# Performance work log

Measured on AMD Instinct MI355X. Metric: run time of the kernel, lower is better.

## Reference

```python
import jax, jax.numpy as jnp
import numpy as np

NUM_HEADS = 16
DIM_K = 64
EMB_DIM = 1024
NEG_INF = -1.0e9


def setup_inputs() -> dict:
    key = jax.random.key(0)
    ks = jax.random.split(key, 12)
    B, Sq, Skv, D = 2, 2048, 2048, EMB_DIM
    HDK = NUM_HEADS * DIM_K
    s = 1.0 / np.sqrt(D)
    return {
        "q": jax.random.normal(ks[0], (B, Sq, D), jnp.float32),
        "k": jax.random.normal(ks[1], (B, Skv, D), jnp.float32),
        "v": jax.random.normal(ks[2], (B, Skv, D), jnp.float32),
        "mask": jax.random.randint(ks[3], (B, 1, Skv), 0, 2, jnp.int32),
        "Wq": jax.random.normal(ks[4], (D, HDK), jnp.float32) * s,
        "bq": jnp.zeros((HDK,), jnp.float32),
        "Wk": jax.random.normal(ks[5], (D, HDK), jnp.float32) * s,
        "bk": jnp.zeros((HDK,), jnp.float32),
        "Wv": jax.random.normal(ks[6], (D, HDK), jnp.float32) * s,
        "bv": jnp.zeros((HDK,), jnp.float32),
        "Wo": jax.random.normal(ks[7], (HDK, D), jnp.float32) * (1.0 / np.sqrt(HDK)),
        "bo": jnp.zeros((D,), jnp.float32),
    }


def reference(q, k, v, mask, Wq, bq, Wk, bk, Wv, bv, Wo, bo):
    B, Sq, _ = q.shape
    Skv = k.shape[1]
    H, dk = NUM_HEADS, DIM_K
    # projections  (B,S,D) -> (B,H,S,dk)
    qh = (q @ Wq + bq).reshape(B, Sq, H, dk).transpose(0, 2, 1, 3)
    kh = (k @ Wk + bk).reshape(B, Skv, H, dk).transpose(0, 2, 1, 3)
    vh = (v @ Wv + bv).reshape(B, Skv, H, dk).transpose(0, 2, 1, 3)
    # scores (B,H,Sq,Skv)
    scores = jnp.einsum("bhqd,bhkd->bhqk", qh, kh) / jnp.float32(np.sqrt(dk))
    # mask (B,1,Skv) -> (B,1,1,Skv); masked_fill where mask == 0
    scores = jnp.where(mask[:, None] == 0, jnp.float32(NEG_INF), scores)
    probs = jax.nn.softmax(scores, axis=-1)  # dropout is identity in eval
    attn = jnp.einsum("bhqk,bhkd->bhqd", probs, vh)
    concat = attn.transpose(0, 2, 1, 3).reshape(B, Sq, H * dk)
    output = concat @ Wo + bo
    return output, scores
```

## Files before the change

kernel.cpp:

```cpp
#include <hip/hip_runtime.h>
#include <hip/hip_bf16.h>

typedef __attribute__((ext_vector_type(8))) short short8;
typedef __attribute__((ext_vector_type(4))) float f32x4;
typedef __hip_bfloat16 bf16;

typedef const void __attribute__((address_space(1))) as1_const_void;
typedef void __attribute__((address_space(3))) as3_void;

static __device__ __forceinline__ void gload_lds16(const bf16* g, bf16* l) {
    __builtin_amdgcn_global_load_lds((as1_const_void*)g, (as3_void*)l, 16, 0, 0);
}

#define NH 16
#define DK 64
#define SEQ 2048
#define DIM 1024
#define NEG_INF_F (-1.0e9f)
#define AST 68

static __device__ __forceinline__ unsigned short f2bf_bits(float f) {
    bf16 t = __float2bfloat16(f);
    return *reinterpret_cast<unsigned short*>(&t);
}

__global__ void cvt_all_kernel(const float* __restrict__ q, const float* __restrict__ k,
                               const float* __restrict__ v, bf16* __restrict__ qb,
                               bf16* __restrict__ kb, bf16* __restrict__ vb) {
    const int N4 = 2 * SEQ * DIM / 4;
    int i = blockIdx.x * blockDim.x + threadIdx.x;
    int sel = i / N4, j = i - sel * N4;
    const float* in = (sel == 0) ? q : (sel == 1) ? k : v;
    bf16* out = (sel == 0) ? qb : (sel == 1) ? kb : vb;
    float4 x = reinterpret_cast<const float4*>(in)[j];
    ushort4 u;
    u.x = f2bf_bits(x.x);
    u.y = f2bf_bits(x.y);
    u.z = f2bf_bits(x.z);
    u.w = f2bf_bits(x.w);
    reinterpret_cast<ushort4*>(out)[j] = u;
}

__global__ void transpose_cvt_kernel(const float* __restrict__ Wq, const float* __restrict__ Wk,
                                     const float* __restrict__ Wv, const float* __restrict__ Wo,
                                     bf16* __restrict__ Wqt, bf16* __restrict__ Wkt,
                                     bf16* __restrict__ Wvt, bf16* __restrict__ Wot) {
    __shared__ float t[32][33];
    const int z = blockIdx.z;
    const float* W = (z == 0) ? Wq : (z == 1) ? Wk : (z == 2) ? Wv : Wo;
    bf16* Wt = (z == 0) ? Wqt : (z == 1) ? Wkt : (z == 2) ? Wvt : Wot;
    int n0 = blockIdx.x * 32, k0 = blockIdx.y * 32;
    int tx = threadIdx.x, ty = threadIdx.y;
#pragma unroll
    for (int i = 0; i < 4; i++)
        t[ty + i * 8][tx] = W[(size_t)(k0 + ty + i * 8) * DIM + n0 + tx];
    __syncthreads();
#pragma unroll
    for (int i = 0; i < 4; i++)
        Wt[(size_t)(n0 + ty + i * 8) * DIM + k0 + tx] = __float2bfloat16(t[tx][ty + i * 8]);
}

__global__ __launch_bounds__(256) void qkv_gemm_kernel(
    const bf16* __restrict__ qb, const bf16* __restrict__ kb, const bf16* __restrict__ vb,
    const bf16* __restrict__ Wcat,
    const float* __restrict__ bq, const float* __restrict__ bk, const float* __restrict__ bv,
    bf16* __restrict__ Qh, bf16* __restrict__ Kh, bf16* __restrict__ Vt)
{
    __shared__ __align__(16) bf16 Xs[2][128 * 32];
    __shared__ __align__(16) bf16 Ws[2][128 * 32];
    const int tid = threadIdx.x;
    const int w = tid >> 6, l = tid & 63;
    const int l15 = l & 15, l4 = l >> 4;
    const int lin = blockIdx.x;
    const int swz = (lin & 7) * 96 + (lin >> 3);
    const int proj = swz >> 8;
    const int rem = swz & 255;
    const int m0 = (rem >> 3) * 128;
    const int n0 = (rem & 7) * 128;
    const bf16* X = (proj == 0) ? qb : (proj == 1) ? kb : vb;
    const bf16* Wt = Wcat + (size_t)proj * DIM * DIM + (size_t)n0 * DIM;
    const float* bias = (proj == 0) ? bq : (proj == 1) ? bk : bv;
    const int wr = w >> 1, wc = w & 1;
    f32x4 acc[4][4] = {};

    const int c0 = tid, c1 = 256 + tid;
    const int r0 = c0 >> 2, ch0 = c0 & 3;
    const int r1 = c1 >> 2, ch1 = c1 & 3;
    const bf16* Xp = X + (size_t)m0 * DIM;

    gload_lds16(&Xp[(size_t)r0 * DIM + ch0 * 8], &Xs[0][c0 * 8]);
    gload_lds16(&Xp[(size_t)r1 * DIM + ch1 * 8], &Xs[0][c1 * 8]);
    gload_lds16(&Wt[(size_t)r0 * DIM + ch0 * 8], &Ws[0][c0 * 8]);
    gload_lds16(&Wt[(size_t)r1 * DIM + ch1 * 8], &Ws[0][c1 * 8]);
    __syncthreads();

    int cur = 0;
    for (int k0 = 0; k0 < DIM; k0 += 32) {
        if (k0 + 32 < DIM) {
            gload_lds16(&Xp[(size_t)r0 * DIM + k0 + 32 + ch0 * 8], &Xs[cur ^ 1][c0 * 8]);
            gload_lds16(&Xp[(size_t)r1 * DIM + k0 + 32 + ch1 * 8], &Xs[cur ^ 1][c1 * 8]);
            gload_lds16(&Wt[(size_t)r0 * DIM + k0 + 32 + ch0 * 8], &Ws[cur ^ 1][c0 * 8]);
            gload_lds16(&Wt[(size_t)r1 * DIM + k0 + 32 + ch1 * 8], &Ws[cur ^ 1][c1 * 8]);
        }
        short8 af[4], bfr[4];
#pragma unroll
        for (int mi = 0; mi < 4; mi++)
            af[mi] = *reinterpret_cast<const short8*>(&Xs[cur][(wr * 64 + mi * 16 + l15) * 32 + l4 * 8]);
#pragma unroll
        for (int ni = 0; ni < 4; ni++)
            bfr[ni] = *reinterpret_cast<const short8*>(&Ws[cur][(wc * 64 + ni * 16 + l15) * 32 + l4 * 8]);
#pragma unroll
        for (int mi = 0; mi < 4; mi++)
#pragma unroll
            for (int ni = 0; ni < 4; ni++)
                acc[mi][ni] = __builtin_amdgcn_mfma_f32_16x16x32_bf16(af[mi], bfr[ni], acc[mi][ni], 0, 0, 0);
        __syncthreads();
        cur ^= 1;
    }

#pragma unroll
    for (int mi = 0; mi < 4; mi++) {
#pragma unroll
        for (int ni = 0; ni < 4; ni++) {
            int n = n0 + wc * 64 + ni * 16 + l15;
            float bv = bias[n];
            int h = n >> 6, d = n & 63;
#pragma unroll
            for (int j = 0; j < 4; j++) {
                int m = m0 + wr * 64 + mi * 16 + l4 * 4 + j;
                float val = acc[mi][ni][j] + bv;
                int b = m >> 11, s = m & 2047;
                if (proj == 0)
                    Qh[((size_t)(b * NH + h) * SEQ + s) * DK + d] = __float2bfloat16(val * 0.125f);
                else if (proj == 1)
                    Kh[((size_t)(b * NH + h) * SEQ + s) * DK + d] = __float2bfloat16(val);
                else
                    Vt[((size_t)(b * NH + h) * DK + d) * SEQ + s] = __float2bfloat16(val);
            }
        }
    }
}

__global__ __launch_bounds__(256) void o_gemm_kernel(
    const bf16* __restrict__ X, const bf16* __restrict__ Wt,
    const float* __restrict__ bias, float* __restrict__ out)
{
    __shared__ __align__(16) bf16 Xs[2][64 * 32];
    __shared__ __align__(16) bf16 Ws[2][128 * 32];
    const int tid = threadIdx.x;
    const int w = tid >> 6, l = tid & 63;
    const int l15 = l & 15, l4 = l >> 4;
    const int lin = blockIdx.x;
    const int swz = (lin & 7) * 64 + (lin >> 3);
    const int m0 = (swz >> 3) * 64;
    const int n0 = (swz & 7) * 128;
    const int wr = w >> 1, wc = w & 1;
    f32x4 acc[2][4] = {};

    const int c0 = tid, c1 = 256 + tid;
    const int r0 = c0 >> 2, ch0 = c0 & 3;
    const int r1 = c1 >> 2, ch1 = c1 & 3;
    const bf16* Xp = X + (size_t)m0 * DIM;
    const bf16* Wp = Wt + (size_t)n0 * DIM;

    gload_lds16(&Xp[(size_t)r0 * DIM + ch0 * 8], &Xs[0][c0 * 8]);
    gload_lds16(&Wp[(size_t)r0 * DIM + ch0 * 8], &Ws[0][c0 * 8]);
    gload_lds16(&Wp[(size_t)r1 * DIM + ch1 * 8], &Ws[0][c1 * 8]);
    __syncthreads();

    int cur = 0;
    for (int k0 = 0; k0 < DIM; k0 += 32) {
        if (k0 + 32 < DIM) {
            gload_lds16(&Xp[(size_t)r0 * DIM + k0 + 32 + ch0 * 8], &Xs[cur ^ 1][c0 * 8]);
            gload_lds16(&Wp[(size_t)r0 * DIM + k0 + 32 + ch0 * 8], &Ws[cur ^ 1][c0 * 8]);
            gload_lds16(&Wp[(size_t)r1 * DIM + k0 + 32 + ch1 * 8], &Ws[cur ^ 1][c1 * 8]);
        }
        short8 af[2], bfr[4];
#pragma unroll
        for (int mi = 0; mi < 2; mi++)
            af[mi] = *reinterpret_cast<const short8*>(&Xs[cur][(wr * 32 + mi * 16 + l15) * 32 + l4 * 8]);
#pragma unroll
        for (int ni = 0; ni < 4; ni++)
            bfr[ni] = *reinterpret_cast<const short8*>(&Ws[cur][(wc * 64 + ni * 16 + l15) * 32 + l4 * 8]);
#pragma unroll
        for (int mi = 0; mi < 2; mi++)
#pragma unroll
            for (int ni = 0; ni < 4; ni++)
                acc[mi][ni] = __builtin_amdgcn_mfma_f32_16x16x32_bf16(af[mi], bfr[ni], acc[mi][ni], 0, 0, 0);
        __syncthreads();
        cur ^= 1;
    }

#pragma unroll
    for (int mi = 0; mi < 2; mi++) {
#pragma unroll
        for (int ni = 0; ni < 4; ni++) {
            int n = n0 + wc * 64 + ni * 16 + l15;
            float bv = bias[n];
#pragma unroll
            for (int j = 0; j < 4; j++) {
                int m = m0 + wr * 32 + mi * 16 + l4 * 4 + j;
                out[(size_t)m * DIM + n] = acc[mi][ni][j] + bv;
            }
        }
    }
}

__global__ __launch_bounds__(256, 3) void attn_kernel(
    const bf16* __restrict__ Qh, const bf16* __restrict__ Kh,
    const bf16* __restrict__ Vt, const int* __restrict__ mask,
    float* __restrict__ scores, bf16* __restrict__ attn_c)
{
    __shared__ __align__(16) bf16 Ks[2][64 * AST];
    __shared__ __align__(16) bf16 Vs[2][64 * AST];
    __shared__ __align__(16) bf16 Ps[128 * AST];
    const int tid = threadIdx.x;
    const int w = tid >> 6, l = tid & 63;
    const int l15 = l & 15, l4 = l >> 4;
    const int lin = blockIdx.x;
    const int swz = (lin & 7) * 64 + (lin >> 3);
    const int bh = swz >> 4;
    const int q0 = (swz & 15) * 128;
    const int b = bh >> 4, h = bh & 15;
    const size_t head = (size_t)bh * SEQ * DK;

    const int c0 = tid, c1 = 256 + tid;
    const int kr0 = c0 >> 3, kc0 = c0 & 7;
    const int kr1 = c1 >> 3, kc1 = c1 & 7;

    const int* mrow = mask + b * SEQ;

    short8 aq[2][2];
#pragma unroll
    for (int mi = 0; mi < 2; mi++)
#pragma unroll
        for (int ks = 0; ks < 2; ks++)
            aq[mi][ks] = *reinterpret_cast<const short8*>(
                &Qh[head + (size_t)(q0 + w * 32 + mi * 16 + l15) * DK + ks * 32 + l4 * 8]);

    {
        short8 k0v = *reinterpret_cast<const short8*>(&Kh[head + (size_t)kr0 * DK + kc0 * 8]);
        short8 k1v = *reinterpret_cast<const short8*>(&Kh[head + (size_t)kr1 * DK + kc1 * 8]);
        short8 v0v = *reinterpret_cast<const short8*>(&Vt[head + (size_t)kr0 * SEQ + kc0 * 8]);
        short8 v1v = *reinterpret_cast<const short8*>(&Vt[head + (size_t)kr1 * SEQ + kc1 * 8]);
        *reinterpret_cast<short8*>(&Ks[0][kr0 * AST + kc0 * 8]) = k0v;
        *reinterpret_cast<short8*>(&Ks[0][kr1 * AST + kc1 * 8]) = k1v;
        *reinterpret_cast<short8*>(&Vs[0][kr0 * AST + kc0 * 8]) = v0v;
        *reinterpret_cast<short8*>(&Vs[0][kr1 * AST + kc1 * 8]) = v1v;
    }
    __syncthreads();

    f32x4 oacc[2][4] = {};
    float mrun[2][4], lrun[2][4];
#pragma unroll
    for (int mi = 0; mi < 2; mi++)
#pragma unroll
        for (int j = 0; j < 4; j++) { mrun[mi][j] = -INFINITY; lrun[mi][j] = 0.f; }

    int cur = 0;
    for (int t = 0; t < SEQ / 64; t++) {
        const int kv0 = t * 64;
        const bool more = t < (SEQ / 64 - 1);
        short8 nk0, nk1, nv0, nv1;
        if (more) {
            nk0 = *reinterpret_cast<const short8*>(&Kh[head + (size_t)(kv0 + 64 + kr0) * DK + kc0 * 8]);
            nk1 = *reinterpret_cast<const short8*>(&Kh[head + (size_t)(kv0 + 64 + kr1) * DK + kc1 * 8]);
            nv0 = *reinterpret_cast<const short8*>(&Vt[head + (size_t)kr0 * SEQ + kv0 + 64 + kc0 * 8]);
            nv1 = *reinterpret_cast<const short8*>(&Vt[head + (size_t)kr1 * SEQ + kv0 + 64 + kc1 * 8]);
        }

        f32x4 sacc[2][4] = {};
#pragma unroll
        for (int ks = 0; ks < 2; ks++) {
            short8 bk[4];
#pragma unroll
            for (int ni = 0; ni < 4; ni++)
                bk[ni] = *reinterpret_cast<const short8*>(&Ks[cur][(ni * 16 + l15) * AST + ks * 32 + l4 * 8]);
#pragma unroll
            for (int mi = 0; mi < 2; mi++)
#pragma unroll
                for (int ni = 0; ni < 4; ni++)
                    sacc[mi][ni] = __builtin_amdgcn_mfma_f32_16x16x32_bf16(aq[mi][ks], bk[ni], sacc[mi][ni], 0, 0, 0);
        }

        int mk[4];
#pragma unroll
        for (int ni = 0; ni < 4; ni++) mk[ni] = mrow[kv0 + ni * 16 + l15];
#pragma unroll
        for (int mi = 0; mi < 2; mi++)
#pragma unroll
            for (int ni = 0; ni < 4; ni++)
                if (mk[ni] == 0) {
#pragma unroll
                    for (int j = 0; j < 4; j++) sacc[mi][ni][j] = NEG_INF_F;
                }

        {
            size_t base = ((size_t)bh * SEQ + q0 + w * 32) * SEQ + kv0;
#pragma unroll
            for (int mi = 0; mi < 2; mi++)
#pragma unroll
                for (int j = 0; j < 4; j++) {
                    size_t rb = base + (size_t)(mi * 16 + l4 * 4 + j) * SEQ;
#pragma unroll
                    for (int ni = 0; ni < 4; ni++)
                        __builtin_nontemporal_store(sacc[mi][ni][j], &scores[rb + ni * 16 + l15]);
                }
        }

#pragma unroll
        for (int mi = 0; mi < 2; mi++)
#pragma unroll
            for (int j = 0; j < 4; j++) {
                float mx = fmaxf(fmaxf(sacc[mi][0][j], sacc[mi][1][j]),
                                 fmaxf(sacc[mi][2][j], sacc[mi][3][j]));
#pragma unroll
                for (int d = 1; d < 16; d <<= 1) mx = fmaxf(mx, __shfl_xor(mx, d));
                if (mx > mrun[mi][j]) {
                    float fac = __expf(mrun[mi][j] - mx);
                    lrun[mi][j] *= fac;
#pragma unroll
                    for (int ni = 0; ni < 4; ni++) oacc[mi][ni][j] *= fac;
                    mrun[mi][j] = mx;
                }
                float mcur = mrun[mi][j];
                float ps = 0.f;
#pragma unroll
                for (int ni = 0; ni < 4; ni++) {
                    float p = __expf(sacc[mi][ni][j] - mcur);
                    sacc[mi][ni][j] = p;
                    ps += p;
                }
                lrun[mi][j] += ps;
            }

#pragma unroll
        for (int mi = 0; mi < 2; mi++)
#pragma unroll
            for (int j = 0; j < 4; j++) {
                int r = w * 32 + mi * 16 + l4 * 4 + j;
#pragma unroll
                for (int ni = 0; ni < 4; ni++)
                    Ps[r * AST + ni * 16 + l15] = __float2bfloat16(sacc[mi][ni][j]);
            }

#pragma unroll
        for (int ks = 0; ks < 2; ks++) {
            short8 pa[2], vbf[4];
#pragma unroll
            for (int mi = 0; mi < 2; mi++)
                pa[mi] = *reinterpret_cast<const short8*>(&Ps[(w * 32 + mi * 16 + l15) * AST + ks * 32 + l4 * 8]);
#pragma unroll
            for (int ni = 0; ni < 4; ni++)
                vbf[ni] = *reinterpret_cast<const short8*>(&Vs[cur][(ni * 16 + l15) * AST + ks * 32 + l4 * 8]);
#pragma unroll
            for (int mi = 0; mi < 2; mi++)
#pragma unroll
                for (int ni = 0; ni < 4; ni++)
                    oacc[mi][ni] = __builtin_amdgcn_mfma_f32_16x16x32_bf16(pa[mi], vbf[ni], oacc[mi][ni], 0, 0, 0);
        }

        if (more) {
            *reinterpret_cast<short8*>(&Ks[cur ^ 1][kr0 * AST + kc0 * 8]) = nk0;
            *reinterpret_cast<short8*>(&Ks[cur ^ 1][kr1 * AST + kc1 * 8]) = nk1;
            *reinterpret_cast<short8*>(&Vs[cur ^ 1][kr0 * AST + kc0 * 8]) = nv0;
            *reinterpret_cast<short8*>(&Vs[cur ^ 1][kr1 * AST + kc1 * 8]) = nv1;
        }
        __syncthreads();
        cur ^= 1;
    }

#pragma unroll
    for (int mi = 0; mi < 2; mi++)
#pragma unroll
        for (int j = 0; j < 4; j++) {
            float ls = lrun[mi][j];
#pragma unroll
            for (int d = 1; d < 16; d <<= 1) ls += __shfl_xor(ls, d);
            float inv = 1.f / ls;
            int s = q0 + w * 32 + mi * 16 + l4 * 4 + j;
#pragma unroll
            for (int ni = 0; ni < 4; ni++)
                attn_c[((size_t)(b * SEQ + s)) * DIM + h * DK + ni * 16 + l15] =
                    __float2bfloat16(oacc[mi][ni][j] * inv);
        }
}

extern "C" void kernel_launch(void* const* d_in, const int* in_sizes, int n_in,
                              void* d_out, int out_size, void* d_ws, size_t ws_size,
                              hipStream_t stream)
{
    const float* q  = (const float*)d_in[0];
    const float* k  = (const float*)d_in[1];
    const float* v  = (const float*)d_in[2];
    const int*  msk = (const int*)d_in[3];
    const float* Wq = (const float*)d_in[4];
    const float* bq = (const float*)d_in[5];
    const float* Wk = (const float*)d_in[6];
    const float* bk = (const float*)d_in[7];
    const float* Wv = (const float*)d_in[8];
    const float* bv = (const float*)d_in[9];
    const float* Wo = (const float*)d_in[10];
    const float* bo = (const float*)d_in[11];

    const size_t MB = 1ull << 20;
    char* ws = (char*)d_ws;
    bf16* qb  = (bf16*)(ws + 0 * MB);
    bf16* kb  = (bf16*)(ws + 8 * MB);
    bf16* vb  = (bf16*)(ws + 16 * MB);
    bf16* Wqt = (bf16*)(ws + 24 * MB);
    bf16* Wkt = (bf16*)(ws + 26 * MB);
    bf16* Wvt = (bf16*)(ws + 28 * MB);
    bf16* Wot = (bf16*)(ws + 30 * MB);
    bf16* QhD = (bf16*)(ws + 32 * MB);
    bf16* KhD = (bf16*)(ws + 40 * MB);
    bf16* VtD = (bf16*)(ws + 48 * MB);
    bf16* att = (bf16*)(ws + 56 * MB);

    float* out = (float*)d_out;
    float* scores = out + (size_t)4096 * 1024;

    cvt_all_kernel<<<3 * 4096, 256, 0, stream>>>(q, k, v, qb, kb, vb);
    transpose_cvt_kernel<<<dim3(32, 32, 4), dim3(32, 8), 0, stream>>>(
        Wq, Wk, Wv, Wo, Wqt, Wkt, Wvt, Wot);

    qkv_gemm_kernel<<<768, 256, 0, stream>>>(qb, kb, vb, Wqt, bq, bk, bv, QhD, KhD, VtD);

    attn_kernel<<<512, 256, 0, stream>>>(QhD, KhD, VtD, msk, scores, att);

    o_gemm_kernel<<<512, 256, 0, stream>>>(att, Wot, bo, out);
}
```

Before: 244.0 us.

## Transpose QK^T MFMA output so each lane owns a row for vectorized softmax

```diff
diff --git a/kernel.cpp b/kernel.cpp
--- a/kernel.cpp
+++ b/kernel.cpp
@@ -206,7 +206,7 @@
     }
 }
 
-__global__ __launch_bounds__(256, 3) void attn_kernel(
+__global__ __launch_bounds__(256) void attn_kernel(
     const bf16* __restrict__ Qh, const bf16* __restrict__ Kh,
     const bf16* __restrict__ Vt, const int* __restrict__ mask,
     float* __restrict__ scores, bf16* __restrict__ attn_c)
@@ -251,11 +251,8 @@
     __syncthreads();
 
     f32x4 oacc[2][4] = {};
-    float mrun[2][4], lrun[2][4];
-#pragma unroll
-    for (int mi = 0; mi < 2; mi++)
-#pragma unroll
-        for (int j = 0; j < 4; j++) { mrun[mi][j] = -INFINITY; lrun[mi][j] = 0.f; }
+    float mrun[2] = { -INFINITY, -INFINITY };
+    float lrun[2] = { 0.f, 0.f };
 
     int cur = 0;
     for (int t = 0; t < SEQ / 64; t++) {
@@ -280,69 +277,96 @@
             for (int mi = 0; mi < 2; mi++)
 #pragma unroll
                 for (int ni = 0; ni < 4; ni++)
-                    sacc[mi][ni] = __builtin_amdgcn_mfma_f32_16x16x32_bf16(aq[mi][ks], bk[ni], sacc[mi][ni], 0, 0, 0);
-        }
-
-        int mk[4];
-#pragma unroll
-        for (int ni = 0; ni < 4; ni++) mk[ni] = mrow[kv0 + ni * 16 + l15];
+                    sacc[mi][ni] = __builtin_amdgcn_mfma_f32_16x16x32_bf16(bk[ni], aq[mi][ks], sacc[mi][ni], 0, 0, 0);
+        }
+
+        int4 mk[4];
+#pragma unroll
+        for (int ni = 0; ni < 4; ni++)
+            mk[ni] = *reinterpret_cast<const int4*>(&mrow[kv0 + ni * 16 + l4 * 4]);
 #pragma unroll
         for (int mi = 0; mi < 2; mi++)
 #pragma unroll
-            for (int ni = 0; ni < 4; ni++)
-                if (mk[ni] == 0) {
-#pragma unroll
-                    for (int j = 0; j < 4; j++) sacc[mi][ni][j] = NEG_INF_F;
+            for (int ni = 0; ni < 4; ni++) {
+                sacc[mi][ni][0] = mk[ni].x ? sacc[mi][ni][0] : NEG_INF_F;
+                sacc[mi][ni][1] = mk[ni].y ? sacc[mi][ni][1] : NEG_INF_F;
+                sacc[mi][ni][2] = mk[ni].z ? sacc[mi][ni][2] : NEG_INF_F;
+                sacc[mi][ni][3] = mk[ni].w ? sacc[mi][ni][3] : NEG_INF_F;
+            }
+
+#pragma unroll
+        for (int mi = 0; mi < 2; mi++) {
+            size_t rb = ((size_t)bh * SEQ + q0 + w * 32 + mi * 16 + l15) * SEQ + kv0;
+#pragma unroll
+            for (int ni = 0; ni < 4; ni++) {
+                f32x4 v4 = sacc[mi][ni];
+                __builtin_nontemporal_store(v4, reinterpret_cast<f32x4*>(&scores[rb + ni * 16 + l4 * 4]));
+            }
+        }
+
+        float rowmax[2];
+#pragma unroll
+        for (int mi = 0; mi < 2; mi++) {
+            f32x4 m4 = sacc[mi][0];
+#pragma unroll
+            for (int c = 0; c < 4; c++) {
+                m4[c] = fmaxf(fmaxf(m4[c], sacc[mi][1][c]), fmaxf(sacc[mi][2][c], sacc[mi][3][c]));
+            }
+            float mx = fmaxf(fmaxf(m4[0], m4[1]), fmaxf(m4[2], m4[3]));
+            mx = fmaxf(mx, __shfl_xor(mx, 16));
+            mx = fmaxf(mx, __shfl_xor(mx, 32));
+            rowmax[mi] = mx;
+        }
+
+        int grew = (rowmax[0] > mrun[0]) || (rowmax[1] > mrun[1]);
+        if (__any(grew)) {
+            float fac[2];
+#pragma unroll
+            for (int mi = 0; mi < 2; mi++) {
+                float mn = fmaxf(mrun[mi], rowmax[mi]);
+                fac[mi] = __expf(mrun[mi] - mn);
+                lrun[mi] *= fac[mi];
+                mrun[mi] = mn;
+            }
+#pragma unroll
+            for (int mi = 0; mi < 2; mi++)
+#pragma unroll
+                for (int j = 0; j < 4; j++) {
+                    float f = __shfl(fac[mi], l4 * 4 + j);
+#pragma unroll
+                    for (int ni = 0; ni < 4; ni++) oacc[mi][ni][j] *= f;
                 }
-
-        {
-            size_t base = ((size_t)bh * SEQ + q0 + w * 32) * SEQ + kv0;
-#pragma unroll
-            for (int mi = 0; mi < 2; mi++)
+        }
+
+#pragma unroll
+        for (int mi = 0; mi < 2; mi++) {
+            float mcur = mrun[mi];
+            f32x4 s4 = {};
+#pragma unroll
+            for (int ni = 0; ni < 4; ni++) {
 #pragma unroll
                 for (int j = 0; j < 4; j++) {
-                    size_t rb = base + (size_t)(mi * 16 + l4 * 4 + j) * SEQ;
-#pragma unroll
-                    for (int ni = 0; ni < 4; ni++)
-                        __builtin_nontemporal_store(sacc[mi][ni][j], &scores[rb + ni * 16 + l15]);
-                }
-        }
-
-#pragma unroll
-        for (int mi = 0; mi < 2; mi++)
-#pragma unroll
-            for (int j = 0; j < 4; j++) {
-                float mx = fmaxf(fmaxf(sacc[mi][0][j], sacc[mi][1][j]),
-                                 fmaxf(sacc[mi][2][j], sacc[mi][3][j]));
-#pragma unroll
-                for (int d = 1; d < 16; d <<= 1) mx = fmaxf(mx, __shfl_xor(mx, d));
-                if (mx > mrun[mi][j]) {
-                    float fac = __expf(mrun[mi][j] - mx);
-                    lrun[mi][j] *= fac;
-#pragma unroll
-                    for (int ni = 0; ni < 4; ni++) oacc[mi][ni][j] *= fac;
-                    mrun[mi][j] = mx;
-                }
-                float mcur = mrun[mi][j];
-                float ps = 0.f;
-#pragma unroll
-                for (int ni = 0; ni < 4; ni++) {
                     float p = __expf(sacc[mi][ni][j] - mcur);
                     sacc[mi][ni][j] = p;
-                    ps += p;
+                    s4[j] += p;
                 }
-                lrun[mi][j] += ps;
-            }
-
-#pragma unroll
-        for (int mi = 0; mi < 2; mi++)
-#pragma unroll
-            for (int j = 0; j < 4; j++) {
-                int r = w * 32 + mi * 16 + l4 * 4 + j;
-#pragma unroll
-                for (int ni = 0; ni < 4; ni++)
-                    Ps[r * AST + ni * 16 + l15] = __float2bfloat16(sacc[mi][ni][j]);
-            }
+            }
+            lrun[mi] += (s4[0] + s4[1]) + (s4[2] + s4[3]);
+        }
+
+#pragma unroll
+        for (int mi = 0; mi < 2; mi++) {
+            int row = w * 32 + mi * 16 + l15;
+#pragma unroll
+            for (int ni = 0; ni < 4; ni++) {
+                ushort4 u;
+                u.x = f2bf_bits(sacc[mi][ni][0]);
+                u.y = f2bf_bits(sacc[mi][ni][1]);
+                u.z = f2bf_bits(sacc[mi][ni][2]);
+                u.w = f2bf_bits(sacc[mi][ni][3]);
+                *reinterpret_cast<ushort4*>(&Ps[row * AST + ni * 16 + l4 * 4]) = u;
+            }
+        }
 
 #pragma unroll
         for (int ks = 0; ks < 2; ks++) {
@@ -371,12 +395,15 @@
     }
 
 #pragma unroll
+    for (int mi = 0; mi < 2; mi++) {
+        lrun[mi] += __shfl_xor(lrun[mi], 16);
+        lrun[mi] += __shfl_xor(lrun[mi], 32);
+    }
+#pragma unroll
     for (int mi = 0; mi < 2; mi++)
 #pragma unroll
         for (int j = 0; j < 4; j++) {
-            float ls = lrun[mi][j];
-#pragma unroll
-            for (int d = 1; d < 16; d <<= 1) ls += __shfl_xor(ls, d);
+            float ls = __shfl(lrun[mi], l4 * 4 + j);
             float inv = 1.f / ls;
             int s = q0 + w * 32 + mi * 16 + l4 * 4 + j;
 #pragma unroll
```

New measurement: 296.5 us. 21.5% more time.

## Restructure attention kernel to 8 waves with 16 rows each and 128-wide KV tiles

Applied to the files above, without the earlier changes.

```diff
diff --git a/kernel.cpp b/kernel.cpp
--- a/kernel.cpp
+++ b/kernel.cpp
@@ -17,7 +17,6 @@
 #define SEQ 2048
 #define DIM 1024
 #define NEG_INF_F (-1.0e9f)
-#define AST 68
 
 static __device__ __forceinline__ unsigned short f2bf_bits(float f) {
     bf16 t = __float2bfloat16(f);
@@ -206,14 +205,14 @@
     }
 }
 
-__global__ __launch_bounds__(256, 3) void attn_kernel(
+__global__ __launch_bounds__(512) void attn_kernel(
     const bf16* __restrict__ Qh, const bf16* __restrict__ Kh,
     const bf16* __restrict__ Vt, const int* __restrict__ mask,
     float* __restrict__ scores, bf16* __restrict__ attn_c)
 {
-    __shared__ __align__(16) bf16 Ks[2][64 * AST];
-    __shared__ __align__(16) bf16 Vs[2][64 * AST];
-    __shared__ __align__(16) bf16 Ps[128 * AST];
+    __shared__ __align__(16) bf16 Ks[2][128 * 68];
+    __shared__ __align__(16) bf16 Vs[2][64 * 132];
+    __shared__ __align__(16) bf16 Ps[128 * 132];
     const int tid = threadIdx.x;
     const int w = tid >> 6, l = tid & 63;
     const int l15 = l & 15, l4 = l >> 4;
@@ -224,166 +223,146 @@
     const int b = bh >> 4, h = bh & 15;
     const size_t head = (size_t)bh * SEQ * DK;
 
-    const int c0 = tid, c1 = 256 + tid;
-    const int kr0 = c0 >> 3, kc0 = c0 & 7;
-    const int kr1 = c1 >> 3, kc1 = c1 & 7;
+    const int ck0 = tid, ck1 = 512 + tid;
+    const int kR0 = ck0 >> 3, kS0 = ck0 & 7;
+    const int kR1 = ck1 >> 3, kS1 = ck1 & 7;
+    const int vR0 = ck0 >> 4, vS0 = ck0 & 15;
+    const int vR1 = ck1 >> 4, vS1 = ck1 & 15;
 
     const int* mrow = mask + b * SEQ;
 
-    short8 aq[2][2];
-#pragma unroll
-    for (int mi = 0; mi < 2; mi++)
-#pragma unroll
-        for (int ks = 0; ks < 2; ks++)
-            aq[mi][ks] = *reinterpret_cast<const short8*>(
-                &Qh[head + (size_t)(q0 + w * 32 + mi * 16 + l15) * DK + ks * 32 + l4 * 8]);
+    short8 aq[2];
+#pragma unroll
+    for (int ks = 0; ks < 2; ks++)
+        aq[ks] = *reinterpret_cast<const short8*>(
+            &Qh[head + (size_t)(q0 + w * 16 + l15) * DK + ks * 32 + l4 * 8]);
 
     {
-        short8 k0v = *reinterpret_cast<const short8*>(&Kh[head + (size_t)kr0 * DK + kc0 * 8]);
-        short8 k1v = *reinterpret_cast<const short8*>(&Kh[head + (size_t)kr1 * DK + kc1 * 8]);
-        short8 v0v = *reinterpret_cast<const short8*>(&Vt[head + (size_t)kr0 * SEQ + kc0 * 8]);
-        short8 v1v = *reinterpret_cast<const short8*>(&Vt[head + (size_t)kr1 * SEQ + kc1 * 8]);
-        *reinterpret_cast<short8*>(&Ks[0][kr0 * AST + kc0 * 8]) = k0v;
-        *reinterpret_cast<short8*>(&Ks[0][kr1 * AST + kc1 * 8]) = k1v;
-        *reinterpret_cast<short8*>(&Vs[0][kr0 * AST + kc0 * 8]) = v0v;
-        *reinterpret_cast<short8*>(&Vs[0][kr1 * AST + kc1 * 8]) = v1v;
+        short8 k0v = *reinterpret_cast<const short8*>(&Kh[head + (size_t)kR0 * DK + kS0 * 8]);
+        short8 k1v = *reinterpret_cast<const short8*>(&Kh[head + (size_t)kR1 * DK + kS1 * 8]);
+        short8 v0v = *reinterpret_cast<const short8*>(&Vt[head + (size_t)vR0 * SEQ + vS0 * 8]);
+        short8 v1v = *reinterpret_cast<const short8*>(&Vt[head + (size_t)vR1 * SEQ + vS1 * 8]);
+        *reinterpret_cast<short8*>(&Ks[0][kR0 * 68 + kS0 * 8]) = k0v;
+        *reinterpret_cast<short8*>(&Ks[0][kR1 * 68 + kS1 * 8]) = k1v;
+        *reinterpret_cast<short8*>(&Vs[0][vR0 * 132 + vS0 * 8]) = v0v;
+        *reinterpret_cast<short8*>(&Vs[0][vR1 * 132 + vS1 * 8]) = v1v;
     }
     __syncthreads();
 
-    f32x4 oacc[2][4] = {};
-    float mrun[2][4], lrun[2][4];
-#pragma unroll
-    for (int mi = 0; mi < 2; mi++)
-#pragma unroll
-        for (int j = 0; j < 4; j++) { mrun[mi][j] = -INFINITY; lrun[mi][j] = 0.f; }
+    f32x4 oacc[4] = {};
+    float mrun[4], lrun[4];
+#pragma unroll
+    for (int j = 0; j < 4; j++) { mrun[j] = -INFINITY; lrun[j] = 0.f; }
 
     int cur = 0;
-    for (int t = 0; t < SEQ / 64; t++) {
-        const int kv0 = t * 64;
-        const bool more = t < (SEQ / 64 - 1);
+    for (int t = 0; t < SEQ / 128; t++) {
+        const int kv0 = t * 128;
+        const bool more = t < (SEQ / 128 - 1);
         short8 nk0, nk1, nv0, nv1;
         if (more) {
-            nk0 = *reinterpret_cast<const short8*>(&Kh[head + (size_t)(kv0 + 64 + kr0) * DK + kc0 * 8]);
-            nk1 = *reinterpret_cast<const short8*>(&Kh[head + (size_t)(kv0 + 64 + kr1) * DK + kc1 * 8]);
-            nv0 = *reinterpret_cast<const short8*>(&Vt[head + (size_t)kr0 * SEQ + kv0 + 64 + kc0 * 8]);
-            nv1 = *reinterpret_cast<const short8*>(&Vt[head + (size_t)kr1 * SEQ + kv0 + 64 + kc1 * 8]);
-        }
-
-        f32x4 sacc[2][4] = {};
+            nk0 = *reinterpret_cast<const short8*>(&Kh[head + (size_t)(kv0 + 128 + kR0) * DK + kS0 * 8]);
+            nk1 = *reinterpret_cast<const short8*>(&Kh[head + (size_t)(kv0 + 128 + kR1) * DK + kS1 * 8]);
+            nv0 = *reinterpret_cast<const short8*>(&Vt[head + (size_t)vR0 * SEQ + kv0 + 128 + vS0 * 8]);
+            nv1 = *reinterpret_cast<const short8*>(&Vt[head + (size_t)vR1 * SEQ + kv0 + 128 + vS1 * 8]);
+        }
+
+        f32x4 sacc[8] = {};
 #pragma unroll
         for (int ks = 0; ks < 2; ks++) {
-            short8 bk[4];
-#pragma unroll
-            for (int ni = 0; ni < 4; ni++)
-                bk[ni] = *reinterpret_cast<const short8*>(&Ks[cur][(ni * 16 + l15) * AST + ks * 32 + l4 * 8]);
-#pragma unroll
-            for (int mi = 0; mi < 2; mi++)
-#pragma unroll
-                for (int ni = 0; ni < 4; ni++)
-                    sacc[mi][ni] = __builtin_amdgcn_mfma_f32_16x16x32_bf16(aq[mi][ks], bk[ni], sacc[mi][ni], 0, 0, 0);
-        }
-
-        int mk[4];
-#pragma unroll
-        for (int ni = 0; ni < 4; ni++) mk[ni] = mrow[kv0 + ni * 16 + l15];
-#pragma unroll
-        for (int mi = 0; mi < 2; mi++)
-#pragma unroll
-            for (int ni = 0; ni < 4; ni++)
-                if (mk[ni] == 0) {
-#pragma unroll
-                    for (int j = 0; j < 4; j++) sacc[mi][ni][j] = NEG_INF_F;
-                }
+#pragma unroll
+            for (int ni = 0; ni < 8; ni++) {
+                short8 bk = *reinterpret_cast<const short8*>(
+                    &Ks[cur][(ni * 16 + l15) * 68 + ks * 32 + l4 * 8]);
+                sacc[ni] = __builtin_amdgcn_mfma_f32_16x16x32_bf16(aq[ks], bk, sacc[ni], 0, 0, 0);
+            }
+        }
+
+#pragma unroll
+        for (int ni = 0; ni < 8; ni++) {
+            int mk = mrow[kv0 + ni * 16 + l15];
+            if (mk == 0) {
+#pragma unroll
+                for (int j = 0; j < 4; j++) sacc[ni][j] = NEG_INF_F;
+            }
+        }
 
         {
-            size_t base = ((size_t)bh * SEQ + q0 + w * 32) * SEQ + kv0;
-#pragma unroll
-            for (int mi = 0; mi < 2; mi++)
-#pragma unroll
-                for (int j = 0; j < 4; j++) {
-                    size_t rb = base + (size_t)(mi * 16 + l4 * 4 + j) * SEQ;
-#pragma unroll
-                    for (int ni = 0; ni < 4; ni++)
-                        __builtin_nontemporal_store(sacc[mi][ni][j], &scores[rb + ni * 16 + l15]);
-                }
-        }
-
-#pragma unroll
-        for (int mi = 0; mi < 2; mi++)
+            size_t base = ((size_t)bh * SEQ + q0 + w * 16) * SEQ + kv0;
 #pragma unroll
             for (int j = 0; j < 4; j++) {
-                float mx = fmaxf(fmaxf(sacc[mi][0][j], sacc[mi][1][j]),
-                                 fmaxf(sacc[mi][2][j], sacc[mi][3][j]));
-#pragma unroll
-                for (int d = 1; d < 16; d <<= 1) mx = fmaxf(mx, __shfl_xor(mx, d));
-                if (mx > mrun[mi][j]) {
-                    float fac = __expf(mrun[mi][j] - mx);
-                    lrun[mi][j] *= fac;
-#pragma unroll
-                    for (int ni = 0; ni < 4; ni++) oacc[mi][ni][j] *= fac;
-                    mrun[mi][j] = mx;
-                }
-                float mcur = mrun[mi][j];
-                float ps = 0.f;
-#pragma unroll
-                for (int ni = 0; ni < 4; ni++) {
-                    float p = __expf(sacc[mi][ni][j] - mcur);
-                    sacc[mi][ni][j] = p;
-                    ps += p;
-                }
-                lrun[mi][j] += ps;
-            }
-
-#pragma unroll
-        for (int mi = 0; mi < 2; mi++)
-#pragma unroll
-            for (int j = 0; j < 4; j++) {
-                int r = w * 32 + mi * 16 + l4 * 4 + j;
-#pragma unroll
-                for (int ni = 0; ni < 4; ni++)
-                    Ps[r * AST + ni * 16 + l15] = __float2bfloat16(sacc[mi][ni][j]);
-            }
-
-#pragma unroll
-        for (int ks = 0; ks < 2; ks++) {
-            short8 pa[2], vbf[4];
-#pragma unroll
-            for (int mi = 0; mi < 2; mi++)
-                pa[mi] = *reinterpret_cast<const short8*>(&Ps[(w * 32 + mi * 16 + l15) * AST + ks * 32 + l4 * 8]);
-#pragma unroll
-            for (int ni = 0; ni < 4; ni++)
-                vbf[ni] = *reinterpret_cast<const short8*>(&Vs[cur][(ni * 16 + l15) * AST + ks * 32 + l4 * 8]);
-#pragma unroll
-            for (int mi = 0; mi < 2; mi++)
-#pragma unroll
-                for (int ni = 0; ni < 4; ni++)
-                    oacc[mi][ni] = __builtin_amdgcn_mfma_f32_16x16x32_bf16(pa[mi], vbf[ni], oacc[mi][ni], 0, 0, 0);
+                size_t rb = base + (size_t)(l4 * 4 + j) * SEQ;
+#pragma unroll
+                for (int ni = 0; ni < 8; ni++)
+                    __builtin_nontemporal_store(sacc[ni][j], &scores[rb + ni * 16 + l15]);
+            }
+        }
+
+#pragma unroll
+        for (int j = 0; j < 4; j++) {
+            float mx = fmaxf(fmaxf(fmaxf(sacc[0][j], sacc[1][j]), fmaxf(sacc[2][j], sacc[3][j])),
+                             fmaxf(fmaxf(sacc[4][j], sacc[5][j]), fmaxf(sacc[6][j], sacc[7][j])));
+#pragma unroll
+            for (int d = 1; d < 16; d <<= 1) mx = fmaxf(mx, __shfl_xor(mx, d));
+            if (mx > mrun[j]) {
+                float fac = __expf(mrun[j] - mx);
+                lrun[j] *= fac;
+#pragma unroll
+                for (int ni = 0; ni < 4; ni++) oacc[ni][j] *= fac;
+                mrun[j] = mx;
+            }
+            float mcur = mrun[j];
+            float ps = 0.f;
+#pragma unroll
+            for (int ni = 0; ni < 8; ni++) {
+                float p = __expf(sacc[ni][j] - mcur);
+                sacc[ni][j] = p;
+                ps += p;
+            }
+            lrun[j] += ps;
+        }
+
+#pragma unroll
+        for (int j = 0; j < 4; j++) {
+            int r = w * 16 + l4 * 4 + j;
+#pragma unroll
+            for (int ni = 0; ni < 8; ni++)
+                Ps[r * 132 + ni * 16 + l15] = __float2bfloat16(sacc[ni][j]);
+        }
+
+#pragma unroll
+        for (int ks = 0; ks < 4; ks++) {
+            short8 pa = *reinterpret_cast<const short8*>(
+                &Ps[(w * 16 + l15) * 132 + ks * 32 + l4 * 8]);
+#pragma unroll
+            for (int ni = 0; ni < 4; ni++) {
+                short8 vbf = *reinterpret_cast<const short8*>(
+                    &Vs[cur][(ni * 16 + l15) * 132 + ks * 32 + l4 * 8]);
+                oacc[ni] = __builtin_amdgcn_mfma_f32_16x16x32_bf16(pa, vbf, oacc[ni], 0, 0, 0);
+            }
         }
 
         if (more) {
-            *reinterpret_cast<short8*>(&Ks[cur ^ 1][kr0 * AST + kc0 * 8]) = nk0;
-            *reinterpret_cast<short8*>(&Ks[cur ^ 1][kr1 * AST + kc1 * 8]) = nk1;
-            *reinterpret_cast<short8*>(&Vs[cur ^ 1][kr0 * AST + kc0 * 8]) = nv0;
-            *reinterpret_cast<short8*>(&Vs[cur ^ 1][kr1 * AST + kc1 * 8]) = nv1;
+            *reinterpret_cast<short8*>(&Ks[cur ^ 1][kR0 * 68 + kS0 * 8]) = nk0;
+            *reinterpret_cast<short8*>(&Ks[cur ^ 1][kR1 * 68 + kS1 * 8]) = nk1;
+            *reinterpret_cast<short8*>(&Vs[cur ^ 1][vR0 * 132 + vS0 * 8]) = nv0;
+            *reinterpret_cast<short8*>(&Vs[cur ^ 1][vR1 * 132 + vS1 * 8]) = nv1;
         }
         __syncthreads();
         cur ^= 1;
     }
 
 #pragma unroll
-    for (int mi = 0; mi < 2; mi++)
-#pragma unroll
-        for (int j = 0; j < 4; j++) {
-            float ls = lrun[mi][j];
-#pragma unroll
-            for (int d = 1; d < 16; d <<= 1) ls += __shfl_xor(ls, d);
-            float inv = 1.f / ls;
-            int s = q0 + w * 32 + mi * 16 + l4 * 4 + j;
-#pragma unroll
-            for (int ni = 0; ni < 4; ni++)
-                attn_c[((size_t)(b * SEQ + s)) * DIM + h * DK + ni * 16 + l15] =
-                    __float2bfloat16(oacc[mi][ni][j] * inv);
-        }
+    for (int j = 0; j < 4; j++) {
+        float ls = lrun[j];
+#pragma unroll
+        for (int d = 1; d < 16; d <<= 1) ls += __shfl_xor(ls, d);
+        float inv = 1.f / ls;
+        int s = q0 + w * 16 + l4 * 4 + j;
+#pragma unroll
+        for (int ni = 0; ni < 4; ni++)
+            attn_c[((size_t)(b * SEQ + s)) * DIM + h * DK + ni * 16 + l15] =
+                __float2bfloat16(oacc[ni][j] * inv);
+    }
 }
 
 extern "C" void kernel_launch(void* const* d_in, const int* in_sizes, int n_in,
@@ -426,7 +405,7 @@
 
     qkv_gemm_kernel<<<768, 256, 0, stream>>>(qb, kb, vb, Wqt, bq, bk, bv, QhD, KhD, VtD);
 
-    attn_kernel<<<512, 256, 0, stream>>>(QhD, KhD, VtD, msk, scores, att);
+    attn_kernel<<<512, 512, 0, stream>>>(QhD, KhD, VtD, msk, scores, att);
 
     o_gemm_kernel<<<512, 256, 0, stream>>>(att, Wot, bo, out);
 }
```

After: 221.3 us. 9.3% less time.
